# Kernel tuning notes

Hardware: AMD Instinct MI355X
Metric: run time of the kernel (lower is better)

Reference implementation:

```python
import jax, jax.numpy as jnp
import numpy as np

N_HEAD = 16
N_EMBD = 1024
B, T = 4, 1024


def setup_inputs() -> dict:
    key = jax.random.key(0)
    ks = jax.random.split(key, 8)
    hs = N_EMBD // N_HEAD
    x = jax.random.normal(ks[0], (B, T, N_EMBD), dtype=jnp.float32)
    # previous-layer attention load per token, ~O(1/T) like a softmax column mean
    refractory_state = jax.random.uniform(ks[1], (B, T), dtype=jnp.float32) / T
    s_attn = 1.0 / np.sqrt(N_EMBD)
    W_attn = jax.random.normal(ks[2], (N_EMBD, 3 * N_EMBD), dtype=jnp.float32) * s_attn
    b_attn = jnp.zeros((3 * N_EMBD,), dtype=jnp.float32)
    W_proj = jax.random.normal(ks[3], (N_EMBD, N_EMBD), dtype=jnp.float32) * s_attn
    b_proj = jnp.zeros((N_EMBD,), dtype=jnp.float32)
    # learnable LIF params, init per module (lif_mode='refractory')
    threshold = jnp.full((N_HEAD,), 0.01, dtype=jnp.float32)
    leak = jnp.full((N_HEAD,), 2.0, dtype=jnp.float32)
    steepness = jnp.full((N_HEAD,), 2.0, dtype=jnp.float32)
    ref_strength = jnp.full((N_HEAD,), -2.0, dtype=jnp.float32)
    cross_w = jnp.full((N_HEAD,), -2.0, dtype=jnp.float32)
    return {
        "x": x, "refractory_state": refractory_state,
        "W_attn": W_attn, "b_attn": b_attn,
        "W_proj": W_proj, "b_proj": b_proj,
        "threshold": threshold, "leak": leak, "steepness": steepness,
        "ref_strength": ref_strength, "cross_w": cross_w,
    }


def reference(x, refractory_state, W_attn, b_attn, W_proj, b_proj,
              threshold, leak, steepness, ref_strength, cross_w):
    Bq, Tq, C = x.shape
    H = N_HEAD
    hs = C // H
    qkv = x @ W_attn + b_attn                     # [B,T,3C]
    q, k, v = jnp.split(qkv, 3, axis=-1)
    q = q.reshape(Bq, Tq, H, hs).transpose(0, 2, 1, 3)  # [B,H,T,hs]
    k = k.reshape(Bq, Tq, H, hs).transpose(0, 2, 1, 3)
    v = v.reshape(Bq, Tq, H, hs).transpose(0, 2, 1, 3)

    att = jnp.einsum('bhqd,bhkd->bhqk', q, k) * (1.0 / jnp.sqrt(jnp.asarray(hs, x.dtype)))
    causal = jnp.tril(jnp.ones((Tq, Tq), dtype=bool))
    att = jnp.where(causal[None, None], att, -jnp.inf)
    probs = jax.nn.softmax(att, axis=-1)          # [B,H,T,T]

    thr = (jnp.abs(threshold) * 0.1)[None, :, None, None]
    lk = jax.nn.sigmoid(leak)[None, :, None, None]
    st = jax.nn.softplus(steepness)[None, :, None, None]
    # refractory: column load over queries + cross-layer load
    column_load = probs.mean(axis=-2, keepdims=True)          # [B,H,1,T]
    eff_thr = thr + jax.nn.softplus(ref_strength)[None, :, None, None] * column_load
    eff_thr = eff_thr + jax.nn.sigmoid(cross_w)[None, :, None, None] * refractory_state[:, None, None, :]

    fire = jax.nn.sigmoid(st * (probs - eff_thr))
    lif_w = fire + lk * (1.0 - fire)
    mod = probs * lif_w
    mod = mod / (mod.sum(axis=-1, keepdims=True) + 1e-8)
    new_refractory = mod.mean(axis=1).mean(axis=-2)           # [B,T]

    y = jnp.einsum('bhqk,bhkd->bhqd', mod, v)
    y = y.transpose(0, 2, 1, 3).reshape(Bq, Tq, C)
    y = y @ W_proj + b_proj
    return y, new_refractory
```

## Files before the change

### kernel.cpp

```cpp
#include <hip/hip_runtime.h>
#include <math.h>

#define B_  4
#define T_  1024
#define C_  1024
#define H_  16
#define HS_ 64
#define K2E 0.1803368801f
#define LOG2E 1.44269504f

typedef _Float16 f16;
typedef _Float16 f16x8 __attribute__((ext_vector_type(8)));
typedef float f32x4 __attribute__((ext_vector_type(4)));

#define MFMA16(a,b,c) __builtin_amdgcn_mfma_f32_16x16x32_f16(a,b,c,0,0,0)
#define EXP2(x) __builtin_amdgcn_exp2f(x)
#define RCP(x)  __builtin_amdgcn_rcpf(x)

__device__ __forceinline__ float qsum_(float v){
    v += __shfl_xor(v,1,64); v += __shfl_xor(v,2,64);
    v += __shfl_xor(v,4,64); v += __shfl_xor(v,8,64);
    return v;
}
__device__ __forceinline__ float sigmoidf_(float x){ return 1.0f/(1.0f + __expf(-x)); }
__device__ __forceinline__ float softplusf_(float x){ return fmaxf(x, 0.0f) + log1pf(__expf(-fabsf(x))); }

__global__ __launch_bounds__(256) void conv_f16_k(
    const float* __restrict__ in, f16* __restrict__ out, int n8)
{
    int i = blockIdx.x*256 + threadIdx.x;
    if (i < n8){
        const float4* p = (const float4*)in + (size_t)i*2;
        float4 a = p[0], b = p[1];
        f16x8 o;
        o[0]=(f16)a.x; o[1]=(f16)a.y; o[2]=(f16)a.z; o[3]=(f16)a.w;
        o[4]=(f16)b.x; o[5]=(f16)b.y; o[6]=(f16)b.z; o[7]=(f16)b.w;
        *((f16x8*)out + i) = o;
    }
}

__global__ __launch_bounds__(256) void transpose_f16_k(
    const float* __restrict__ in, f16* __restrict__ out, int K, int N)
{
    __shared__ float tl[32][33];
    const int n0 = blockIdx.x*32, k0 = blockIdx.y*32;
    const int c = threadIdx.x & 31, r4 = threadIdx.x >> 5;
    #pragma unroll
    for (int i=0;i<4;i++){
        int r = r4*4 + i;
        tl[r][c] = in[(size_t)(k0+r)*N + n0 + c];
    }
    __syncthreads();
    #pragma unroll
    for (int i=0;i<4;i++){
        int r = r4*4 + i;
        out[(size_t)(n0+r)*K + k0 + c] = (f16)tl[c][r];
    }
}

#define CT_STRIDE 132
__global__ __launch_bounds__(256) void gemm_qkv_k(
    const f16* __restrict__ A, const f16* __restrict__ Bt,
    const float* __restrict__ bias,
    f16* __restrict__ Qh, f16* __restrict__ Kh, f16* __restrict__ Vt)
{
    __shared__ __align__(16) f16 smem[128*CT_STRIDE];
    f16* Al = smem;
    f16* Bl = smem + 4096;
    f16* Ct = smem;
    const int tid = threadIdx.x;
    const int lane = tid & 63, wave = tid >> 6;
    const int lx = lane & 15, quad = lane >> 4;
    const int wm = wave & 1, wn = wave >> 1;
    const int m0 = blockIdx.y*128, n0 = blockIdx.x*128;
    f32x4 acc[4][4];
    #pragma unroll
    for (int i=0;i<4;i++){
        #pragma unroll
        for (int j=0;j<4;j++){ acc[i][j][0]=0.f;acc[i][j][1]=0.f;acc[i][j][2]=0.f;acc[i][j][3]=0.f; }
    }
    f16x8 ra[2], rb[2];
    #pragma unroll
    for (int i=0;i<2;i++){
        int c = i*4 + wave;
        ra[i] = *(const f16x8*)(A  + (size_t)(m0 + c*16 + lx)*1024 + quad*8);
        rb[i] = *(const f16x8*)(Bt + (size_t)(n0 + c*16 + lx)*1024 + quad*8);
    }
    for (int k0=0; k0<1024; k0+=32){
        __syncthreads();
        #pragma unroll
        for (int i=0;i<2;i++){
            int c = i*4 + wave;
            *(f16x8*)&Al[c*512 + quad*128 + lx*8] = ra[i];
            *(f16x8*)&Bl[c*512 + quad*128 + lx*8] = rb[i];
        }
        __syncthreads();
        if (k0 + 32 < 1024){
            #pragma unroll
            for (int i=0;i<2;i++){
                int c = i*4 + wave;
                ra[i] = *(const f16x8*)(A  + (size_t)(m0 + c*16 + lx)*1024 + k0+32 + quad*8);
                rb[i] = *(const f16x8*)(Bt + (size_t)(n0 + c*16 + lx)*1024 + k0+32 + quad*8);
            }
        }
        f16x8 af[4], bf[4];
        #pragma unroll
        for (int mt=0;mt<4;mt++) af[mt] = *(const f16x8*)&Al[(wm*4+mt)*512 + quad*128 + lx*8];
        #pragma unroll
        for (int nt=0;nt<4;nt++) bf[nt] = *(const f16x8*)&Bl[(wn*4+nt)*512 + quad*128 + lx*8];
        #pragma unroll
        for (int mt=0;mt<4;mt++){
            #pragma unroll
            for (int nt=0;nt<4;nt++)
                acc[mt][nt] = MFMA16(af[mt], bf[nt], acc[mt][nt]);
        }
    }
    __syncthreads();
    #pragma unroll
    for (int mt=0;mt<4;mt++){
        #pragma unroll
        for (int nt=0;nt<4;nt++){
            int n_loc = wn*64 + nt*16 + lx;
            float bv = bias[n0 + n_loc];
            #pragma unroll
            for (int r=0;r<4;r++){
                int m_loc = wm*64 + mt*16 + quad*4 + r;
                Ct[m_loc*CT_STRIDE + n_loc] = (f16)(acc[mt][nt][r] + bv);
            }
        }
    }
    __syncthreads();
    const int bb = m0 >> 10;
    if (n0 < 2048){
        for (int it=0; it<8; it++){
            int row = it*32 + wave*8 + (lane>>3);
            int ch  = lane & 7;
            int m_loc = row >> 1, half = row & 1;
            f16x8 v = *(const f16x8*)&Ct[m_loc*CT_STRIDE + half*64 + ch*8];
            int n = n0 + half*64;
            int which = n >> 10, cc = n & 1023, h = cc >> 6;
            int t = (m0 + m_loc) & 1023;
            f16* dst = (which==0) ? Qh : Kh;
            *(f16x8*)(dst + ((size_t)(bb*16+h)*1024 + t)*64 + ch*8) = v;
        }
    } else {
        for (int it=0; it<8; it++){
            int drow = it*16 + wave*4 + (lane>>4);
            int ch   = lane & 15;
            int cc = (n0 + drow) & 1023;
            int h = cc >> 6, d = cc & 63;
            f16 tmp[8];
            #pragma unroll
            for (int j=0;j<8;j++) tmp[j] = Ct[(ch*8+j)*CT_STRIDE + drow];
            int t = (m0 + ch*8) & 1023;
            *(f16x8*)(Vt + ((size_t)(bb*16+h)*64 + d)*1024 + t) = *(f16x8*)tmp;
        }
    }
}

__global__ __launch_bounds__(256) void gemm_proj_k(
    const f16* __restrict__ A, const f16* __restrict__ Bt,
    const float* __restrict__ bias, float* __restrict__ out)
{
    __shared__ __align__(16) f16 Al[8*512];
    __shared__ __align__(16) f16 Bl[4*512];
    const int tid = threadIdx.x;
    const int lane = tid & 63, wave = tid >> 6;
    const int lx = lane & 15, quad = lane >> 4;
    const int wm = wave & 1, wn = wave >> 1;
    const int m0 = blockIdx.y*128, n0 = blockIdx.x*64;
    f32x4 acc[4][2];
    #pragma unroll
    for (int i=0;i<4;i++){
        #pragma unroll
        for (int j=0;j<2;j++){ acc[i][j][0]=0.f;acc[i][j][1]=0.f;acc[i][j][2]=0.f;acc[i][j][3]=0.f; }
    }
    f16x8 ra[2], rb;
    #pragma unroll
    for (int i=0;i<2;i++)
        ra[i] = *(const f16x8*)(A + (size_t)(m0 + (i*4+wave)*16 + lx)*1024 + quad*8);
    rb = *(const f16x8*)(Bt + (size_t)(n0 + wave*16 + lx)*1024 + quad*8);
    for (int k0=0; k0<1024; k0+=32){
        __syncthreads();
        #pragma unroll
        for (int i=0;i<2;i++)
            *(f16x8*)&Al[(i*4+wave)*512 + quad*128 + lx*8] = ra[i];
        *(f16x8*)&Bl[wave*512 + quad*128 + lx*8] = rb;
        __syncthreads();
        if (k0 + 32 < 1024){
            #pragma unroll
            for (int i=0;i<2;i++)
                ra[i] = *(const f16x8*)(A + (size_t)(m0 + (i*4+wave)*16 + lx)*1024 + k0+32 + quad*8);
            rb = *(const f16x8*)(Bt + (size_t)(n0 + wave*16 + lx)*1024 + k0+32 + quad*8);
        }
        f16x8 af[4], bf[2];
        #pragma unroll
        for (int mt=0;mt<4;mt++) af[mt] = *(const f16x8*)&Al[(wm*4+mt)*512 + quad*128 + lx*8];
        #pragma unroll
        for (int nt=0;nt<2;nt++) bf[nt] = *(const f16x8*)&Bl[(wn*2+nt)*512 + quad*128 + lx*8];
        #pragma unroll
        for (int mt=0;mt<4;mt++){
            #pragma unroll
            for (int nt=0;nt<2;nt++)
                acc[mt][nt] = MFMA16(af[mt], bf[nt], acc[mt][nt]);
        }
    }
    #pragma unroll
    for (int mt=0;mt<4;mt++){
        #pragma unroll
        for (int nt=0;nt<2;nt++){
            int n = n0 + wn*32 + nt*16 + lx;
            float bv = bias[n];
            #pragma unroll
            for (int r=0;r<4;r++){
                int m = m0 + wm*64 + mt*16 + quad*4 + r;
                out[(size_t)m*1024 + n] = acc[mt][nt][r] + bv;
            }
        }
    }
}

__global__ __launch_bounds__(256) void attn_stats_k(
    const f16* __restrict__ Qh, const f16* __restrict__ Kh,
    float* __restrict__ rowl, float* __restrict__ colp)
{
    __shared__ __align__(16) f16 Kl[4096];
    __shared__ float colacc[64];
    const int tid = threadIdx.x;
    const int lane = tid & 63, wave = tid >> 6;
    const int lx = lane & 15, quad = lane >> 4;
    const int g  = 15 - (blockIdx.x >> 6);
    const int bh = blockIdx.x & 63;
    const int qpos = wave*16 + quad*4;
    const size_t kbase = (size_t)bh*1024*64;

    const size_t qoff = ((size_t)bh*1024 + g*64 + wave*16 + lx)*64;
    f16x8 aq0 = *(const f16x8*)(Qh + qoff + quad*8);
    f16x8 aq1 = *(const f16x8*)(Qh + qoff + 32 + quad*8);

    f16x8 rk[2];
    #pragma unroll
    for (int i=0;i<2;i++){
        int u = i*4+wave, c = u&3, kh = u>>2;
        rk[i] = *(const f16x8*)(Kh + kbase + (size_t)(c*16+lx)*64 + kh*32 + quad*8);
    }

    float ls[4] = {0.f,0.f,0.f,0.f};
    for (int kt=0; kt<=g; kt++){
        __syncthreads();
        #pragma unroll
        for (int i=0;i<2;i++){
            int u = i*4+wave, c = u&3, kh = u>>2;
            *(f16x8*)&Kl[c*1024 + kh*512 + quad*128 + lx*8] = rk[i];
        }
        __syncthreads();
        if (kt < g){
            #pragma unroll
            for (int i=0;i<2;i++){
                int u = i*4+wave, c = u&3, kh = u>>2;
                rk[i] = *(const f16x8*)(Kh + kbase + (size_t)((kt+1)*64 + c*16+lx)*64 + kh*32 + quad*8);
            }
        }
        const bool diag = (kt == g);
        #pragma unroll
        for (int nt=0;nt<4;nt++){
            f32x4 sc = {0.f,0.f,0.f,0.f};
            f16x8 b0 = *(const f16x8*)&Kl[nt*1024 + quad*128 + lx*8];
            f16x8 b1 = *(const f16x8*)&Kl[nt*1024 + 512 + quad*128 + lx*8];
            sc = MFMA16(aq0, b0, sc);
            sc = MFMA16(aq1, b1, sc);
            #pragma unroll
            for (int r=0;r<4;r++){
                float sv = sc[r];
                if (diag && (nt*16+lx) > (qpos + r)) sv = -1e4f;
                ls[r] += EXP2(sv*K2E);
            }
        }
    }
    float invl[4];
    #pragma unroll
    for (int r=0;r<4;r++){
        float l = qsum_(ls[r]);
        if (lx == 0) rowl[(size_t)bh*1024 + g*64 + qpos + r] = l;
        invl[r] = RCP(l);
    }

    #pragma unroll
    for (int i=0;i<2;i++){
        int u = i*4+wave, c = u&3, kh = u>>2;
        rk[i] = *(const f16x8*)(Kh + kbase + (size_t)(c*16+lx)*64 + kh*32 + quad*8);
    }
    for (int kt=0; kt<=g; kt++){
        __syncthreads();
        #pragma unroll
        for (int i=0;i<2;i++){
            int u = i*4+wave, c = u&3, kh = u>>2;
            *(f16x8*)&Kl[c*1024 + kh*512 + quad*128 + lx*8] = rk[i];
        }
        if (tid < 64) colacc[tid] = 0.f;
        __syncthreads();
        if (kt < g){
            #pragma unroll
            for (int i=0;i<2;i++){
                int u = i*4+wave, c = u&3, kh = u>>2;
                rk[i] = *(const f16x8*)(Kh + kbase + (size_t)((kt+1)*64 + c*16+lx)*64 + kh*32 + quad*8);
            }
        }
        const bool diag = (kt == g);
        #pragma unroll
        for (int nt=0;nt<4;nt++){
            f32x4 sc = {0.f,0.f,0.f,0.f};
            f16x8 b0 = *(const f16x8*)&Kl[nt*1024 + quad*128 + lx*8];
            f16x8 b1 = *(const f16x8*)&Kl[nt*1024 + 512 + quad*128 + lx*8];
            sc = MFMA16(aq0, b0, sc);
            sc = MFMA16(aq1, b1, sc);
            float csum = 0.f;
            #pragma unroll
            for (int r=0;r<4;r++){
                float sv = sc[r];
                if (diag && (nt*16+lx) > (qpos + r)) sv = -1e4f;
                csum += EXP2(sv*K2E) * invl[r];
            }
            csum += __shfl_xor(csum,16,64); csum += __shfl_xor(csum,32,64);
            if (quad == 0) atomicAdd(&colacc[nt*16+lx], csum);
        }
        __syncthreads();
        if (tid < 64) atomicAdd(&colp[(size_t)bh*1024 + kt*64 + tid], colacc[tid]);
    }
}

__global__ __launch_bounds__(256) void attn_apply_k(
    const f16* __restrict__ Qh, const f16* __restrict__ Kh, const f16* __restrict__ Vt,
    const float* __restrict__ rowl,
    const float* __restrict__ colp, const float* __restrict__ refr,
    const float* __restrict__ threshold, const float* __restrict__ leak,
    const float* __restrict__ steepness, const float* __restrict__ ref_strength,
    const float* __restrict__ cross_w,
    f16* __restrict__ Yh, float* __restrict__ racc)
{
    __shared__ __align__(16) f16 Kl[4096];
    __shared__ __align__(16) f16 Vl[4096];
    __shared__ __align__(16) f16 Pl[4][16*72];
    __shared__ float eb[1024];
    __shared__ float colacc[64];
    const int tid = threadIdx.x;
    const int lane = tid & 63, wave = tid >> 6;
    const int lx = lane & 15, quad = lane >> 4;
    const int g  = 15 - (blockIdx.x >> 6);
    const int bh = blockIdx.x & 63;
    const int b  = bh >> 4, h = bh & 15;
    const int qpos = wave*16 + quad*4;
    const size_t kbase = (size_t)bh*1024*64;

    const float thr = fabsf(threshold[h])*0.1f;
    const float lk  = sigmoidf_(leak[h]);
    const float st2 = softplusf_(steepness[h]) * LOG2E;
    const float sprT= softplusf_(ref_strength[h]) * (1.0f/T_);
    const float cw  = sigmoidf_(cross_w[h]);
    const float Alk = 1.f - lk;

    {
        float4 cp = *(const float4*)(colp + (size_t)bh*1024 + tid*4);
        float4 rf = *(const float4*)(refr + (size_t)b*1024 + tid*4);
        eb[tid*4+0] = thr + sprT*cp.x + cw*rf.x;
        eb[tid*4+1] = thr + sprT*cp.y + cw*rf.y;
        eb[tid*4+2] = thr + sprT*cp.z + cw*rf.z;
        eb[tid*4+3] = thr + sprT*cp.w + cw*rf.w;
    }

    const size_t qoff = ((size_t)bh*1024 + g*64 + wave*16 + lx)*64;
    f16x8 aq0 = *(const f16x8*)(Qh + qoff + quad*8);
    f16x8 aq1 = *(const f16x8*)(Qh + qoff + 32 + quad*8);

    float invl[4];
    #pragma unroll
    for (int r=0;r<4;r++)
        invl[r] = RCP(rowl[(size_t)bh*1024 + g*64 + qpos + r]);

    f32x4 y[4];
    #pragma unroll
    for (int i=0;i<4;i++){ y[i][0]=0.f;y[i][1]=0.f;y[i][2]=0.f;y[i][3]=0.f; }
    float Dp[4] = {0.f,0.f,0.f,0.f};

    f16x8 rk[2], rv[2];
    #pragma unroll
    for (int i=0;i<2;i++){
        int u = i*4+wave, c = u&3, kh = u>>2;
        rk[i] = *(const f16x8*)(Kh + kbase + (size_t)(c*16+lx)*64 + kh*32 + quad*8);
        rv[i] = *(const f16x8*)(Vt + kbase + (size_t)(c*16+lx)*1024 + kh*32 + quad*8);
    }

    for (int kt=0; kt<=g; kt++){
        __syncthreads();
        #pragma unroll
        for (int i=0;i<2;i++){
            int u = i*4+wave, c = u&3, kh = u>>2;
            *(f16x8*)&Kl[c*1024 + kh*512 + quad*128 + lx*8] = rk[i];
            *(f16x8*)&Vl[c*1024 + kh*512 + quad*128 + lx*8] = rv[i];
        }
        __syncthreads();
        if (kt < g){
            #pragma unroll
            for (int i=0;i<2;i++){
                int u = i*4+wave, c = u&3, kh = u>>2;
                rk[i] = *(const f16x8*)(Kh + kbase + (size_t)((kt+1)*64 + c*16+lx)*64 + kh*32 + quad*8);
                rv[i] = *(const f16x8*)(Vt + kbase + (size_t)(c*16+lx)*1024 + (kt+1)*64 + kh*32 + quad*8);
            }
        }
        const bool diag = (kt == g);
        #pragma unroll
        for (int nt=0;nt<4;nt++){
            f32x4 sc = {0.f,0.f,0.f,0.f};
            f16x8 b0 = *(const f16x8*)&Kl[nt*1024 + quad*128 + lx*8];
            f16x8 b1 = *(const f16x8*)&Kl[nt*1024 + 512 + quad*128 + lx*8];
            sc = MFMA16(aq0, b0, sc);
            sc = MFMA16(aq1, b1, sc);
            float ec = st2 * eb[kt*64 + nt*16 + lx];
            #pragma unroll
            for (int r=0;r<4;r++){
                float sv = sc[r];
                if (diag && (nt*16+lx) > (qpos + r)) sv = -1e4f;
                float p = EXP2(sv*K2E) * invl[r];
                float e2 = EXP2(ec - st2*p);
                float fire = RCP(1.f + e2);
                float pw = p * (lk + Alk*fire);
                Dp[r] += pw;
                Pl[wave][(quad*4+r)*72 + nt*16 + lx] = (f16)pw;
            }
        }
        f16x8 ap0 = *(const f16x8*)&Pl[wave][lx*72 + quad*8];
        f16x8 ap1 = *(const f16x8*)&Pl[wave][lx*72 + 32 + quad*8];
        #pragma unroll
        for (int dt=0;dt<4;dt++){
            f16x8 bv0 = *(const f16x8*)&Vl[dt*1024 + quad*128 + lx*8];
            f16x8 bv1 = *(const f16x8*)&Vl[dt*1024 + 512 + quad*128 + lx*8];
            y[dt] = MFMA16(ap0, bv0, y[dt]);
            y[dt] = MFMA16(ap1, bv1, y[dt]);
        }
    }
    float invD[4];
    #pragma unroll
    for (int r=0;r<4;r++) invD[r] = RCP(qsum_(Dp[r]) + 1e-8f);
    #pragma unroll
    for (int dt=0;dt<4;dt++){
        #pragma unroll
        for (int r=0;r<4;r++)
            Pl[wave][(quad*4+r)*72 + dt*16 + lx] = (f16)(y[dt][r]*invD[r]);
    }
    #pragma unroll
    for (int it=0; it<2; it++){
        int q = it*8 + (lane>>3), ch = lane & 7;
        f16x8 v = *(const f16x8*)&Pl[wave][q*72 + ch*8];
        *(f16x8*)(Yh + (size_t)(b*1024 + g*64 + wave*16 + q)*1024 + h*64 + ch*8) = v;
    }

    #pragma unroll
    for (int i=0;i<2;i++){
        int u = i*4+wave, c = u&3, kh = u>>2;
        rk[i] = *(const f16x8*)(Kh + kbase + (size_t)(c*16+lx)*64 + kh*32 + quad*8);
    }
    for (int kt=0; kt<=g; kt++){
        __syncthreads();
        #pragma unroll
        for (int i=0;i<2;i++){
            int u = i*4+wave, c = u&3, kh = u>>2;
            *(f16x8*)&Kl[c*1024 + kh*512 + quad*128 + lx*8] = rk[i];
        }
        if (tid < 64) colacc[tid] = 0.f;
        __syncthreads();
        if (kt < g){
            #pragma unroll
            for (int i=0;i<2;i++){
                int u = i*4+wave, c = u&3, kh = u>>2;
                rk[i] = *(const f16x8*)(Kh + kbase + (size_t)((kt+1)*64 + c*16+lx)*64 + kh*32 + quad*8);
            }
        }
        const bool diag = (kt == g);
        #pragma unroll
        for (int nt=0;nt<4;nt++){
            f32x4 sc = {0.f,0.f,0.f,0.f};
            f16x8 b0 = *(const f16x8*)&Kl[nt*1024 + quad*128 + lx*8];
            f16x8 b1 = *(const f16x8*)&Kl[nt*1024 + 512 + quad*128 + lx*8];
            sc = MFMA16(aq0, b0, sc);
            sc = MFMA16(aq1, b1, sc);
            float ec = st2 * eb[kt*64 + nt*16 + lx];
            float csum = 0.f;
            #pragma unroll
            for (int r=0;r<4;r++){
                float sv = sc[r];
                if (diag && (nt*16+lx) > (qpos + r)) sv = -1e4f;
                float p = EXP2(sv*K2E) * invl[r];
                float e2 = EXP2(ec - st2*p);
                float fire = RCP(1.f + e2);
                csum += p * (lk + Alk*fire) * invD[r];
            }
            csum += __shfl_xor(csum,16,64); csum += __shfl_xor(csum,32,64);
            if (quad == 0) atomicAdd(&colacc[nt*16+lx], csum);
        }
        __syncthreads();
        if (tid < 64) atomicAdd(&racc[(size_t)b*1024 + kt*64 + tid], colacc[tid]);
    }
}

__global__ __launch_bounds__(256) void finish_refr_k(
    const float* __restrict__ racc, float* __restrict__ out)
{
    int i = blockIdx.x*256 + threadIdx.x;
    if (i < B_*T_) out[i] = racc[i] * (1.0f/(H_*T_));
}

extern "C" void kernel_launch(void* const* d_in, const int* in_sizes, int n_in,
                              void* d_out, int out_size, void* d_ws, size_t ws_size,
                              hipStream_t stream) {
    (void)in_sizes; (void)n_in; (void)out_size; (void)ws_size;
    const float* x           = (const float*)d_in[0];
    const float* refr        = (const float*)d_in[1];
    const float* W_attn      = (const float*)d_in[2];
    const float* b_attn      = (const float*)d_in[3];
    const float* W_proj      = (const float*)d_in[4];
    const float* b_proj      = (const float*)d_in[5];
    const float* threshold   = (const float*)d_in[6];
    const float* leak        = (const float*)d_in[7];
    const float* steepness   = (const float*)d_in[8];
    const float* ref_strength= (const float*)d_in[9];
    const float* cross_w     = (const float*)d_in[10];
    float* out = (float*)d_out;

    char* ws = (char*)d_ws;
    f16* x_h = (f16*)ws;                       ws += (size_t)4096*1024*2;
    f16* WaT = (f16*)ws;                       ws += (size_t)3072*1024*2;
    f16* WpT = (f16*)ws;                       ws += (size_t)1024*1024*2;
    f16* Qh  = (f16*)ws;                       ws += (size_t)64*1024*64*2;
    f16* Kh  = (f16*)ws;                       ws += (size_t)64*1024*64*2;
    f16* Vt  = (f16*)ws;                       ws += (size_t)64*64*1024*2;
    f16* Yh  = (f16*)ws;                       ws += (size_t)4096*1024*2;
    float* rowl = (float*)ws;                  ws += (size_t)65536*4;
    float* colp = (float*)ws;                  ws += (size_t)65536*4;
    float* racc = (float*)ws;                  ws += (size_t)4096*4;

    hipMemsetAsync(colp, 0, 65536*sizeof(float), stream);
    hipMemsetAsync(racc, 0, 4096*sizeof(float), stream);

    conv_f16_k<<<dim3(2048), dim3(256), 0, stream>>>(x, x_h, 4096*1024/8);
    transpose_f16_k<<<dim3(96,32), dim3(256), 0, stream>>>(W_attn, WaT, 1024, 3072);
    transpose_f16_k<<<dim3(32,32), dim3(256), 0, stream>>>(W_proj, WpT, 1024, 1024);
    gemm_qkv_k<<<dim3(24,32), dim3(256), 0, stream>>>(x_h, WaT, b_attn, Qh, Kh, Vt);
    attn_stats_k<<<dim3(1024), dim3(256), 0, stream>>>(Qh, Kh, rowl, colp);
    attn_apply_k<<<dim3(1024), dim3(256), 0, stream>>>(
        Qh, Kh, Vt, rowl, colp, refr,
        threshold, leak, steepness, ref_strength, cross_w, Yh, racc);
    gemm_proj_k<<<dim3(16,32), dim3(256), 0, stream>>>(Yh, WpT, b_proj, out);
    finish_refr_k<<<dim3(16), dim3(256), 0, stream>>>(racc, out + (size_t)B_*T_*C_);
}
```

Before: 289.8 us.

## Double-buffer LDS tiles, fuse prep kernels, and batch column atomics

Merges the conversion, both weight transposes and the workspace zeroing into one prep kernel, replacing two memsets and three launches. The finish kernel is folded into the projection GEMM as an extra block. The GEMMs and attention loops now double-buffer their LDS tiles with two-deep register prefetch, cutting syncs per iteration from two to one. Per-block column sums go into a full-length shared accumulator and are flushed to global atomics once at the end instead of every tile. The costs are more LDS per block, which may reduce occupancy, and the fused proj kernel reads racc without any visible ordering guarantee relative to attn_apply, though stream order should cover it.

```diff
diff --git a/kernel.cpp b/kernel.cpp
--- a/kernel.cpp
+++ b/kernel.cpp
@@ -25,36 +25,44 @@
 __device__ __forceinline__ float sigmoidf_(float x){ return 1.0f/(1.0f + __expf(-x)); }
 __device__ __forceinline__ float softplusf_(float x){ return fmaxf(x, 0.0f) + log1pf(__expf(-fabsf(x))); }
 
-__global__ __launch_bounds__(256) void conv_f16_k(
-    const float* __restrict__ in, f16* __restrict__ out, int n8)
+__global__ __launch_bounds__(256) void prep_k(
+    const float* __restrict__ x, const float* __restrict__ Wa,
+    const float* __restrict__ Wp,
+    f16* __restrict__ x_h, f16* __restrict__ WaT, f16* __restrict__ WpT,
+    float* __restrict__ zbase)
 {
-    int i = blockIdx.x*256 + threadIdx.x;
-    if (i < n8){
-        const float4* p = (const float4*)in + (size_t)i*2;
+    __shared__ float tl[32][33];
+    const int bid = blockIdx.x, tid = threadIdx.x;
+    if (bid < 2048){
+        int i = bid*256 + tid;
+        const float4* p = (const float4*)x + (size_t)i*2;
         float4 a = p[0], b = p[1];
         f16x8 o;
         o[0]=(f16)a.x; o[1]=(f16)a.y; o[2]=(f16)a.z; o[3]=(f16)a.w;
         o[4]=(f16)b.x; o[5]=(f16)b.y; o[6]=(f16)b.z; o[7]=(f16)b.w;
-        *((f16x8*)out + i) = o;
-    }
-}
-
-__global__ __launch_bounds__(256) void transpose_f16_k(
-    const float* __restrict__ in, f16* __restrict__ out, int K, int N)
-{
-    __shared__ float tl[32][33];
-    const int n0 = blockIdx.x*32, k0 = blockIdx.y*32;
-    const int c = threadIdx.x & 31, r4 = threadIdx.x >> 5;
-    #pragma unroll
-    for (int i=0;i<4;i++){
-        int r = r4*4 + i;
-        tl[r][c] = in[(size_t)(k0+r)*N + n0 + c];
-    }
-    __syncthreads();
-    #pragma unroll
-    for (int i=0;i<4;i++){
-        int r = r4*4 + i;
-        out[(size_t)(n0+r)*K + k0 + c] = (f16)tl[c][r];
+        *((f16x8*)x_h + i) = o;
+    } else if (bid < 5120){
+        int t = bid - 2048;
+        int n0 = (t % 96)*32, k0 = (t / 96)*32;
+        const int c = tid & 31, r4 = tid >> 5;
+        #pragma unroll
+        for (int i=0;i<4;i++){ int r = r4*4+i; tl[r][c] = Wa[(size_t)(k0+r)*3072 + n0 + c]; }
+        __syncthreads();
+        #pragma unroll
+        for (int i=0;i<4;i++){ int r = r4*4+i; WaT[(size_t)(n0+r)*1024 + k0 + c] = (f16)tl[c][r]; }
+    } else if (bid < 6144){
+        int t = bid - 5120;
+        int n0 = (t & 31)*32, k0 = (t >> 5)*32;
+        const int c = tid & 31, r4 = tid >> 5;
+        #pragma unroll
+        for (int i=0;i<4;i++){ int r = r4*4+i; tl[r][c] = Wp[(size_t)(k0+r)*1024 + n0 + c]; }
+        __syncthreads();
+        #pragma unroll
+        for (int i=0;i<4;i++){ int r = r4*4+i; WpT[(size_t)(n0+r)*1024 + k0 + c] = (f16)tl[c][r]; }
+    } else {
+        int idx = (bid - 6144)*256 + tid;
+        float4 z; z.x=0.f; z.y=0.f; z.z=0.f; z.w=0.f;
+        ((float4*)zbase)[idx] = z;
     }
 }
 
@@ -64,58 +72,72 @@
     const float* __restrict__ bias,
     f16* __restrict__ Qh, f16* __restrict__ Kh, f16* __restrict__ Vt)
 {
-    __shared__ __align__(16) f16 smem[128*CT_STRIDE];
-    f16* Al = smem;
-    f16* Bl = smem + 4096;
-    f16* Ct = smem;
+    __shared__ __align__(16) f16 smem[16896];
     const int tid = threadIdx.x;
     const int lane = tid & 63, wave = tid >> 6;
     const int lx = lane & 15, quad = lane >> 4;
     const int wm = wave & 1, wn = wave >> 1;
     const int m0 = blockIdx.y*128, n0 = blockIdx.x*128;
+    const f16* Ap = A  + (size_t)m0*1024;
+    const f16* Bp = Bt + (size_t)n0*1024;
     f32x4 acc[4][4];
     #pragma unroll
     for (int i=0;i<4;i++){
         #pragma unroll
         for (int j=0;j<4;j++){ acc[i][j][0]=0.f;acc[i][j][1]=0.f;acc[i][j][2]=0.f;acc[i][j][3]=0.f; }
     }
-    f16x8 ra[2], rb[2];
+    f16x8 ra[2][2], rb[2][2];
     #pragma unroll
     for (int i=0;i<2;i++){
         int c = i*4 + wave;
-        ra[i] = *(const f16x8*)(A  + (size_t)(m0 + c*16 + lx)*1024 + quad*8);
-        rb[i] = *(const f16x8*)(Bt + (size_t)(n0 + c*16 + lx)*1024 + quad*8);
-    }
-    for (int k0=0; k0<1024; k0+=32){
-        __syncthreads();
-        #pragma unroll
-        for (int i=0;i<2;i++){
-            int c = i*4 + wave;
-            *(f16x8*)&Al[c*512 + quad*128 + lx*8] = ra[i];
-            *(f16x8*)&Bl[c*512 + quad*128 + lx*8] = rb[i];
-        }
-        __syncthreads();
-        if (k0 + 32 < 1024){
+        ra[0][i] = *(const f16x8*)(Ap + (size_t)(c*16+lx)*1024 + quad*8);
+        rb[0][i] = *(const f16x8*)(Bp + (size_t)(c*16+lx)*1024 + quad*8);
+    }
+    #pragma unroll
+    for (int i=0;i<2;i++){
+        int c = i*4 + wave;
+        *(f16x8*)&smem[c*512 + quad*128 + lx*8]        = ra[0][i];
+        *(f16x8*)&smem[4096 + c*512 + quad*128 + lx*8] = rb[0][i];
+    }
+    #pragma unroll
+    for (int i=0;i<2;i++){
+        int c = i*4 + wave;
+        ra[1][i] = *(const f16x8*)(Ap + (size_t)(c*16+lx)*1024 + 32 + quad*8);
+        rb[1][i] = *(const f16x8*)(Bp + (size_t)(c*16+lx)*1024 + 32 + quad*8);
+    }
+    __syncthreads();
+    for (int it=0; it<32; it++){
+        const int cur = (it&1)*8192, nxt = 8192 - cur, s = it&1;
+        if (it < 30){
             #pragma unroll
             for (int i=0;i<2;i++){
                 int c = i*4 + wave;
-                ra[i] = *(const f16x8*)(A  + (size_t)(m0 + c*16 + lx)*1024 + k0+32 + quad*8);
-                rb[i] = *(const f16x8*)(Bt + (size_t)(n0 + c*16 + lx)*1024 + k0+32 + quad*8);
+                ra[s][i] = *(const f16x8*)(Ap + (size_t)(c*16+lx)*1024 + (it+2)*32 + quad*8);
+                rb[s][i] = *(const f16x8*)(Bp + (size_t)(c*16+lx)*1024 + (it+2)*32 + quad*8);
+            }
+        }
+        if (it < 31){
+            #pragma unroll
+            for (int i=0;i<2;i++){
+                int c = i*4 + wave;
+                *(f16x8*)&smem[nxt + c*512 + quad*128 + lx*8]        = ra[s^1][i];
+                *(f16x8*)&smem[nxt + 4096 + c*512 + quad*128 + lx*8] = rb[s^1][i];
             }
         }
         f16x8 af[4], bf[4];
         #pragma unroll
-        for (int mt=0;mt<4;mt++) af[mt] = *(const f16x8*)&Al[(wm*4+mt)*512 + quad*128 + lx*8];
-        #pragma unroll
-        for (int nt=0;nt<4;nt++) bf[nt] = *(const f16x8*)&Bl[(wn*4+nt)*512 + quad*128 + lx*8];
+        for (int mt=0;mt<4;mt++) af[mt] = *(const f16x8*)&smem[cur + (wm*4+mt)*512 + quad*128 + lx*8];
+        #pragma unroll
+        for (int nt=0;nt<4;nt++) bf[nt] = *(const f16x8*)&smem[cur + 4096 + (wn*4+nt)*512 + quad*128 + lx*8];
         #pragma unroll
         for (int mt=0;mt<4;mt++){
             #pragma unroll
             for (int nt=0;nt<4;nt++)
                 acc[mt][nt] = MFMA16(af[mt], bf[nt], acc[mt][nt]);
         }
-    }
-    __syncthreads();
+        __syncthreads();
+    }
+    f16* Ct = smem;
     #pragma unroll
     for (int mt=0;mt<4;mt++){
         #pragma unroll
@@ -160,50 +182,72 @@
 
 __global__ __launch_bounds__(256) void gemm_proj_k(
     const f16* __restrict__ A, const f16* __restrict__ Bt,
-    const float* __restrict__ bias, float* __restrict__ out)
+    const float* __restrict__ bias, float* __restrict__ out,
+    const float* __restrict__ racc)
 {
-    __shared__ __align__(16) f16 Al[8*512];
-    __shared__ __align__(16) f16 Bl[4*512];
+    if (blockIdx.x == 512){
+        float* oref = out + (size_t)B_*T_*C_;
+        #pragma unroll
+        for (int j=0;j<16;j++){
+            int idx = j*256 + threadIdx.x;
+            oref[idx] = racc[idx] * (1.0f/(H_*T_));
+        }
+        return;
+    }
+    __shared__ __align__(16) f16 smem[12288];
     const int tid = threadIdx.x;
     const int lane = tid & 63, wave = tid >> 6;
     const int lx = lane & 15, quad = lane >> 4;
     const int wm = wave & 1, wn = wave >> 1;
-    const int m0 = blockIdx.y*128, n0 = blockIdx.x*64;
+    const int m0 = (blockIdx.x >> 4)*128, n0 = (blockIdx.x & 15)*64;
+    const f16* Ap = A  + (size_t)m0*1024;
+    const f16* Bp = Bt + (size_t)n0*1024;
     f32x4 acc[4][2];
     #pragma unroll
     for (int i=0;i<4;i++){
         #pragma unroll
         for (int j=0;j<2;j++){ acc[i][j][0]=0.f;acc[i][j][1]=0.f;acc[i][j][2]=0.f;acc[i][j][3]=0.f; }
     }
-    f16x8 ra[2], rb;
+    f16x8 ra[2][2], rb[2];
     #pragma unroll
     for (int i=0;i<2;i++)
-        ra[i] = *(const f16x8*)(A + (size_t)(m0 + (i*4+wave)*16 + lx)*1024 + quad*8);
-    rb = *(const f16x8*)(Bt + (size_t)(n0 + wave*16 + lx)*1024 + quad*8);
-    for (int k0=0; k0<1024; k0+=32){
-        __syncthreads();
-        #pragma unroll
-        for (int i=0;i<2;i++)
-            *(f16x8*)&Al[(i*4+wave)*512 + quad*128 + lx*8] = ra[i];
-        *(f16x8*)&Bl[wave*512 + quad*128 + lx*8] = rb;
-        __syncthreads();
-        if (k0 + 32 < 1024){
+        ra[0][i] = *(const f16x8*)(Ap + (size_t)((i*4+wave)*16+lx)*1024 + quad*8);
+    rb[0] = *(const f16x8*)(Bp + (size_t)(wave*16+lx)*1024 + quad*8);
+    #pragma unroll
+    for (int i=0;i<2;i++)
+        *(f16x8*)&smem[(i*4+wave)*512 + quad*128 + lx*8] = ra[0][i];
+    *(f16x8*)&smem[4096 + wave*512 + quad*128 + lx*8] = rb[0];
+    #pragma unroll
+    for (int i=0;i<2;i++)
+        ra[1][i] = *(const f16x8*)(Ap + (size_t)((i*4+wave)*16+lx)*1024 + 32 + quad*8);
+    rb[1] = *(const f16x8*)(Bp + (size_t)(wave*16+lx)*1024 + 32 + quad*8);
+    __syncthreads();
+    for (int it=0; it<32; it++){
+        const int cur = (it&1)*6144, nxt = 6144 - cur, s = it&1;
+        if (it < 30){
             #pragma unroll
             for (int i=0;i<2;i++)
-                ra[i] = *(const f16x8*)(A + (size_t)(m0 + (i*4+wave)*16 + lx)*1024 + k0+32 + quad*8);
-            rb = *(const f16x8*)(Bt + (size_t)(n0 + wave*16 + lx)*1024 + k0+32 + quad*8);
+                ra[s][i] = *(const f16x8*)(Ap + (size_t)((i*4+wave)*16+lx)*1024 + (it+2)*32 + quad*8);
+            rb[s] = *(const f16x8*)(Bp + (size_t)(wave*16+lx)*1024 + (it+2)*32 + quad*8);
+        }
+        if (it < 31){
+            #pragma unroll
+            for (int i=0;i<2;i++)
+                *(f16x8*)&smem[nxt + (i*4+wave)*512 + quad*128 + lx*8] = ra[s^1][i];
+            *(f16x8*)&smem[nxt + 4096 + wave*512 + quad*128 + lx*8] = rb[s^1];
         }
         f16x8 af[4], bf[2];
         #pragma unroll
-        for (int mt=0;mt<4;mt++) af[mt] = *(const f16x8*)&Al[(wm*4+mt)*512 + quad*128 + lx*8];
-        #pragma unroll
-        for (int nt=0;nt<2;nt++) bf[nt] = *(const f16x8*)&Bl[(wn*2+nt)*512 + quad*128 + lx*8];
+        for (int mt=0;mt<4;mt++) af[mt] = *(const f16x8*)&smem[cur + (wm*4+mt)*512 + quad*128 + lx*8];
+        #pragma unroll
+        for (int nt=0;nt<2;nt++) bf[nt] = *(const f16x8*)&smem[cur + 4096 + (wn*2+nt)*512 + quad*128 + lx*8];
         #pragma unroll
         for (int mt=0;mt<4;mt++){
             #pragma unroll
             for (int nt=0;nt<2;nt++)
                 acc[mt][nt] = MFMA16(af[mt], bf[nt], acc[mt][nt]);
         }
+        __syncthreads();
     }
     #pragma unroll
     for (int mt=0;mt<4;mt++){
@@ -224,49 +268,54 @@
     const f16* __restrict__ Qh, const f16* __restrict__ Kh,
     float* __restrict__ rowl, float* __restrict__ colp)
 {
-    __shared__ __align__(16) f16 Kl[4096];
-    __shared__ float colacc[64];
+    __shared__ __align__(16) f16 Kl[8192];
+    __shared__ float cacc[1024];
     const int tid = threadIdx.x;
     const int lane = tid & 63, wave = tid >> 6;
     const int lx = lane & 15, quad = lane >> 4;
     const int g  = 15 - (blockIdx.x >> 6);
     const int bh = blockIdx.x & 63;
     const int qpos = wave*16 + quad*4;
-    const size_t kbase = (size_t)bh*1024*64;
+    const size_t kbase = (size_t)bh*65536;
+
+    for (int i=tid; i<1024; i+=256) cacc[i] = 0.f;
 
     const size_t qoff = ((size_t)bh*1024 + g*64 + wave*16 + lx)*64;
     f16x8 aq0 = *(const f16x8*)(Qh + qoff + quad*8);
     f16x8 aq1 = *(const f16x8*)(Qh + qoff + 32 + quad*8);
 
-    f16x8 rk[2];
-    #pragma unroll
-    for (int i=0;i<2;i++){
-        int u = i*4+wave, c = u&3, kh = u>>2;
-        rk[i] = *(const f16x8*)(Kh + kbase + (size_t)(c*16+lx)*64 + kh*32 + quad*8);
-    }
-
+    f16x8 rk[2][2];
+    #pragma unroll
+    for (int i=0;i<2;i++){ int u=i*4+wave, cc=u&3, kh=u>>2;
+        rk[0][i] = *(const f16x8*)(Kh + kbase + (size_t)(cc*16+lx)*64 + kh*32 + quad*8); }
+    #pragma unroll
+    for (int i=0;i<2;i++){ int u=i*4+wave, cc=u&3, kh=u>>2;
+        *(f16x8*)&Kl[cc*1024 + kh*512 + quad*128 + lx*8] = rk[0][i]; }
+    if (g >= 1){
+        #pragma unroll
+        for (int i=0;i<2;i++){ int u=i*4+wave, cc=u&3, kh=u>>2;
+            rk[1][i] = *(const f16x8*)(Kh + kbase + (size_t)(64 + cc*16+lx)*64 + kh*32 + quad*8); }
+    }
+    __syncthreads();
     float ls[4] = {0.f,0.f,0.f,0.f};
     for (int kt=0; kt<=g; kt++){
-        __syncthreads();
-        #pragma unroll
-        for (int i=0;i<2;i++){
-            int u = i*4+wave, c = u&3, kh = u>>2;
-            *(f16x8*)&Kl[c*1024 + kh*512 + quad*128 + lx*8] = rk[i];
-        }
-        __syncthreads();
-        if (kt < g){
-            #pragma unroll
-            for (int i=0;i<2;i++){
-                int u = i*4+wave, c = u&3, kh = u>>2;
-                rk[i] = *(const f16x8*)(Kh + kbase + (size_t)((kt+1)*64 + c*16+lx)*64 + kh*32 + quad*8);
-            }
+        const int cur = (kt&1)*4096, nxt = 4096 - cur, s = kt&1;
+        if (kt+2 <= g){
+            #pragma unroll
+            for (int i=0;i<2;i++){ int u=i*4+wave, cc=u&3, kh=u>>2;
+                rk[s][i] = *(const f16x8*)(Kh + kbase + (size_t)((kt+2)*64 + cc*16+lx)*64 + kh*32 + quad*8); }
+        }
+        if (kt+1 <= g){
+            #pragma unroll
+            for (int i=0;i<2;i++){ int u=i*4+wave, cc=u&3, kh=u>>2;
+                *(f16x8*)&Kl[nxt + cc*1024 + kh*512 + quad*128 + lx*8] = rk[s^1][i]; }
         }
         const bool diag = (kt == g);
         #pragma unroll
         for (int nt=0;nt<4;nt++){
             f32x4 sc = {0.f,0.f,0.f,0.f};
-            f16x8 b0 = *(const f16x8*)&Kl[nt*1024 + quad*128 + lx*8];
-            f16x8 b1 = *(const f16x8*)&Kl[nt*1024 + 512 + quad*128 + lx*8];
+            f16x8 b0 = *(const f16x8*)&Kl[cur + nt*1024 + quad*128 + lx*8];
+            f16x8 b1 = *(const f16x8*)&Kl[cur + nt*1024 + 512 + quad*128 + lx*8];
             sc = MFMA16(aq0, b0, sc);
             sc = MFMA16(aq1, b1, sc);
             #pragma unroll
@@ -276,6 +325,7 @@
                 ls[r] += EXP2(sv*K2E);
             }
         }
+        __syncthreads();
     }
     float invl[4];
     #pragma unroll
@@ -284,34 +334,36 @@
         if (lx == 0) rowl[(size_t)bh*1024 + g*64 + qpos + r] = l;
         invl[r] = RCP(l);
     }
-
-    #pragma unroll
-    for (int i=0;i<2;i++){
-        int u = i*4+wave, c = u&3, kh = u>>2;
-        rk[i] = *(const f16x8*)(Kh + kbase + (size_t)(c*16+lx)*64 + kh*32 + quad*8);
-    }
+    #pragma unroll
+    for (int i=0;i<2;i++){ int u=i*4+wave, cc=u&3, kh=u>>2;
+        rk[0][i] = *(const f16x8*)(Kh + kbase + (size_t)(cc*16+lx)*64 + kh*32 + quad*8); }
+    #pragma unroll
+    for (int i=0;i<2;i++){ int u=i*4+wave, cc=u&3, kh=u>>2;
+        *(f16x8*)&Kl[cc*1024 + kh*512 + quad*128 + lx*8] = rk[0][i]; }
+    if (g >= 1){
+        #pragma unroll
+        for (int i=0;i<2;i++){ int u=i*4+wave, cc=u&3, kh=u>>2;
+            rk[1][i] = *(const f16x8*)(Kh + kbase + (size_t)(64 + cc*16+lx)*64 + kh*32 + quad*8); }
+    }
+    __syncthreads();
     for (int kt=0; kt<=g; kt++){
-        __syncthreads();
-        #pragma unroll
-        for (int i=0;i<2;i++){
-            int u = i*4+wave, c = u&3, kh = u>>2;
-            *(f16x8*)&Kl[c*1024 + kh*512 + quad*128 + lx*8] = rk[i];
-        }
-        if (tid < 64) colacc[tid] = 0.f;
-        __syncthreads();
-        if (kt < g){
-            #pragma unroll
-            for (int i=0;i<2;i++){
-                int u = i*4+wave, c = u&3, kh = u>>2;
-                rk[i] = *(const f16x8*)(Kh + kbase + (size_t)((kt+1)*64 + c*16+lx)*64 + kh*32 + quad*8);
-            }
+        const int cur = (kt&1)*4096, nxt = 4096 - cur, s = kt&1;
+        if (kt+2 <= g){
+            #pragma unroll
+            for (int i=0;i<2;i++){ int u=i*4+wave, cc=u&3, kh=u>>2;
+                rk[s][i] = *(const f16x8*)(Kh + kbase + (size_t)((kt+2)*64 + cc*16+lx)*64 + kh*32 + quad*8); }
+        }
+        if (kt+1 <= g){
+            #pragma unroll
+            for (int i=0;i<2;i++){ int u=i*4+wave, cc=u&3, kh=u>>2;
+                *(f16x8*)&Kl[nxt + cc*1024 + kh*512 + quad*128 + lx*8] = rk[s^1][i]; }
         }
         const bool diag = (kt == g);
         #pragma unroll
         for (int nt=0;nt<4;nt++){
             f32x4 sc = {0.f,0.f,0.f,0.f};
-            f16x8 b0 = *(const f16x8*)&Kl[nt*1024 + quad*128 + lx*8];
-            f16x8 b1 = *(const f16x8*)&Kl[nt*1024 + 512 + quad*128 + lx*8];
+            f16x8 b0 = *(const f16x8*)&Kl[cur + nt*1024 + quad*128 + lx*8];
+            f16x8 b1 = *(const f16x8*)&Kl[cur + nt*1024 + 512 + quad*128 + lx*8];
             sc = MFMA16(aq0, b0, sc);
             sc = MFMA16(aq1, b1, sc);
             float csum = 0.f;
@@ -322,11 +374,12 @@
                 csum += EXP2(sv*K2E) * invl[r];
             }
             csum += __shfl_xor(csum,16,64); csum += __shfl_xor(csum,32,64);
-            if (quad == 0) atomicAdd(&colacc[nt*16+lx], csum);
-        }
-        __syncthreads();
-        if (tid < 64) atomicAdd(&colp[(size_t)bh*1024 + kt*64 + tid], colacc[tid]);
-    }
+            if (quad == 0) atomicAdd(&cacc[kt*64 + nt*16 + lx], csum);
+        }
+        __syncthreads();
+    }
+    for (int i=tid; i<(g+1)*64; i+=256)
+        atomicAdd(&colp[(size_t)bh*1024 + i], cacc[i]);
 }
 
 __global__ __launch_bounds__(256) void attn_apply_k(
@@ -338,11 +391,11 @@
     const float* __restrict__ cross_w,
     f16* __restrict__ Yh, float* __restrict__ racc)
 {
-    __shared__ __align__(16) f16 Kl[4096];
-    __shared__ __align__(16) f16 Vl[4096];
+    __shared__ __align__(16) f16 Kl[8192];
+    __shared__ __align__(16) f16 Vl[8192];
     __shared__ __align__(16) f16 Pl[4][16*72];
     __shared__ float eb[1024];
-    __shared__ float colacc[64];
+    __shared__ float cacc[1024];
     const int tid = threadIdx.x;
     const int lane = tid & 63, wave = tid >> 6;
     const int lx = lane & 15, quad = lane >> 4;
@@ -350,7 +403,7 @@
     const int bh = blockIdx.x & 63;
     const int b  = bh >> 4, h = bh & 15;
     const int qpos = wave*16 + quad*4;
-    const size_t kbase = (size_t)bh*1024*64;
+    const size_t kbase = (size_t)bh*65536;
 
     const float thr = fabsf(threshold[h])*0.1f;
     const float lk  = sigmoidf_(leak[h]);
@@ -362,11 +415,12 @@
     {
         float4 cp = *(const float4*)(colp + (size_t)bh*1024 + tid*4);
         float4 rf = *(const float4*)(refr + (size_t)b*1024 + tid*4);
-        eb[tid*4+0] = thr + sprT*cp.x + cw*rf.x;
-        eb[tid*4+1] = thr + sprT*cp.y + cw*rf.y;
-        eb[tid*4+2] = thr + sprT*cp.z + cw*rf.z;
-        eb[tid*4+3] = thr + sprT*cp.w + cw*rf.w;
-    }
+        eb[tid*4+0] = st2*(thr + sprT*cp.x + cw*rf.x);
+        eb[tid*4+1] = st2*(thr + sprT*cp.y + cw*rf.y);
+        eb[tid*4+2] = st2*(thr + sprT*cp.z + cw*rf.z);
+        eb[tid*4+3] = st2*(thr + sprT*cp.w + cw*rf.w);
+    }
+    for (int i=tid; i<1024; i+=256) cacc[i] = 0.f;
 
     const size_t qoff = ((size_t)bh*1024 + g*64 + wave*16 + lx)*64;
     f16x8 aq0 = *(const f16x8*)(Qh + qoff + quad*8);
@@ -382,47 +436,51 @@
     for (int i=0;i<4;i++){ y[i][0]=0.f;y[i][1]=0.f;y[i][2]=0.f;y[i][3]=0.f; }
     float Dp[4] = {0.f,0.f,0.f,0.f};
 
-    f16x8 rk[2], rv[2];
-    #pragma unroll
-    for (int i=0;i<2;i++){
-        int u = i*4+wave, c = u&3, kh = u>>2;
-        rk[i] = *(const f16x8*)(Kh + kbase + (size_t)(c*16+lx)*64 + kh*32 + quad*8);
-        rv[i] = *(const f16x8*)(Vt + kbase + (size_t)(c*16+lx)*1024 + kh*32 + quad*8);
-    }
-
+    f16x8 rk[2][2], rv[2][2];
+    #pragma unroll
+    for (int i=0;i<2;i++){ int u=i*4+wave, cc=u&3, kh=u>>2;
+        rk[0][i] = *(const f16x8*)(Kh + kbase + (size_t)(cc*16+lx)*64 + kh*32 + quad*8);
+        rv[0][i] = *(const f16x8*)(Vt + kbase + (size_t)(cc*16+lx)*1024 + kh*32 + quad*8); }
+    #pragma unroll
+    for (int i=0;i<2;i++){ int u=i*4+wave, cc=u&3, kh=u>>2;
+        *(f16x8*)&Kl[cc*1024 + kh*512 + quad*128 + lx*8] = rk[0][i];
+        *(f16x8*)&Vl[cc*1024 + kh*512 + quad*128 + lx*8] = rv[0][i]; }
+    if (g >= 1){
+        #pragma unroll
+        for (int i=0;i<2;i++){ int u=i*4+wave, cc=u&3, kh=u>>2;
+            rk[1][i] = *(const f16x8*)(Kh + kbase + (size_t)(64 + cc*16+lx)*64 + kh*32 + quad*8);
+            rv[1][i] = *(const f16x8*)(Vt + kbase + (size_t)(cc*16+lx)*1024 + 64 + kh*32 + quad*8); }
+    }
+    __syncthreads();
     for (int kt=0; kt<=g; kt++){
-        __syncthreads();
-        #pragma unroll
-        for (int i=0;i<2;i++){
-            int u = i*4+wave, c = u&3, kh = u>>2;
-            *(f16x8*)&Kl[c*1024 + kh*512 + quad*128 + lx*8] = rk[i];
-            *(f16x8*)&Vl[c*1024 + kh*512 + quad*128 + lx*8] = rv[i];
-        }
-        __syncthreads();
-        if (kt < g){
-            #pragma unroll
-            for (int i=0;i<2;i++){
-                int u = i*4+wave, c = u&3, kh = u>>2;
-                rk[i] = *(const f16x8*)(Kh + kbase + (size_t)((kt+1)*64 + c*16+lx)*64 + kh*32 + quad*8);
-                rv[i] = *(const f16x8*)(Vt + kbase + (size_t)(c*16+lx)*1024 + (kt+1)*64 + kh*32 + quad*8);
-            }
+        const int cur = (kt&1)*4096, nxt = 4096 - cur, s = kt&1;
+        if (kt+2 <= g){
+            #pragma unroll
+            for (int i=0;i<2;i++){ int u=i*4+wave, cc=u&3, kh=u>>2;
+                rk[s][i] = *(const f16x8*)(Kh + kbase + (size_t)((kt+2)*64 + cc*16+lx)*64 + kh*32 + quad*8);
+                rv[s][i] = *(const f16x8*)(Vt + kbase + (size_t)(cc*16+lx)*1024 + (kt+2)*64 + kh*32 + quad*8); }
+        }
+        if (kt+1 <= g){
+            #pragma unroll
+            for (int i=0;i<2;i++){ int u=i*4+wave, cc=u&3, kh=u>>2;
+                *(f16x8*)&Kl[nxt + cc*1024 + kh*512 + quad*128 + lx*8] = rk[s^1][i];
+                *(f16x8*)&Vl[nxt + cc*1024 + kh*512 + quad*128 + lx*8] = rv[s^1][i]; }
         }
         const bool diag = (kt == g);
         #pragma unroll
         for (int nt=0;nt<4;nt++){
             f32x4 sc = {0.f,0.f,0.f,0.f};
-            f16x8 b0 = *(const f16x8*)&Kl[nt*1024 + quad*128 + lx*8];
-            f16x8 b1 = *(const f16x8*)&Kl[nt*1024 + 512 + quad*128 + lx*8];
+            f16x8 b0 = *(const f16x8*)&Kl[cur + nt*1024 + quad*128 + lx*8];
+            f16x8 b1 = *(const f16x8*)&Kl[cur + nt*1024 + 512 + quad*128 + lx*8];
             sc = MFMA16(aq0, b0, sc);
             sc = MFMA16(aq1, b1, sc);
-            float ec = st2 * eb[kt*64 + nt*16 + lx];
+            float ec = eb[kt*64 + nt*16 + lx];
             #pragma unroll
             for (int r=0;r<4;r++){
                 float sv = sc[r];
                 if (diag && (nt*16+lx) > (qpos + r)) sv = -1e4f;
                 float p = EXP2(sv*K2E) * invl[r];
-                float e2 = EXP2(ec - st2*p);
-                float fire = RCP(1.f + e2);
+                float fire = RCP(1.f + EXP2(ec - st2*p));
                 float pw = p * (lk + Alk*fire);
                 Dp[r] += pw;
                 Pl[wave][(quad*4+r)*72 + nt*16 + lx] = (f16)pw;
@@ -432,11 +490,12 @@
         f16x8 ap1 = *(const f16x8*)&Pl[wave][lx*72 + 32 + quad*8];
         #pragma unroll
         for (int dt=0;dt<4;dt++){
-            f16x8 bv0 = *(const f16x8*)&Vl[dt*1024 + quad*128 + lx*8];
-            f16x8 bv1 = *(const f16x8*)&Vl[dt*1024 + 512 + quad*128 + lx*8];
+            f16x8 bv0 = *(const f16x8*)&Vl[cur + dt*1024 + quad*128 + lx*8];
+            f16x8 bv1 = *(const f16x8*)&Vl[cur + dt*1024 + 512 + quad*128 + lx*8];
             y[dt] = MFMA16(ap0, bv0, y[dt]);
             y[dt] = MFMA16(ap1, bv1, y[dt]);
         }
+        __syncthreads();
     }
     float invD[4];
     #pragma unroll
@@ -455,58 +514,54 @@
     }
 
     #pragma unroll
-    for (int i=0;i<2;i++){
-        int u = i*4+wave, c = u&3, kh = u>>2;
-        rk[i] = *(const f16x8*)(Kh + kbase + (size_t)(c*16+lx)*64 + kh*32 + quad*8);
-    }
+    for (int i=0;i<2;i++){ int u=i*4+wave, cc=u&3, kh=u>>2;
+        rk[0][i] = *(const f16x8*)(Kh + kbase + (size_t)(cc*16+lx)*64 + kh*32 + quad*8); }
+    #pragma unroll
+    for (int i=0;i<2;i++){ int u=i*4+wave, cc=u&3, kh=u>>2;
+        *(f16x8*)&Kl[cc*1024 + kh*512 + quad*128 + lx*8] = rk[0][i]; }
+    if (g >= 1){
+        #pragma unroll
+        for (int i=0;i<2;i++){ int u=i*4+wave, cc=u&3, kh=u>>2;
+            rk[1][i] = *(const f16x8*)(Kh + kbase + (size_t)(64 + cc*16+lx)*64 + kh*32 + quad*8); }
+    }
+    __syncthreads();
     for (int kt=0; kt<=g; kt++){
-        __syncthreads();
-        #pragma unroll
-        for (int i=0;i<2;i++){
-            int u = i*4+wave, c = u&3, kh = u>>2;
-            *(f16x8*)&Kl[c*1024 + kh*512 + quad*128 + lx*8] = rk[i];
-        }
-        if (tid < 64) colacc[tid] = 0.f;
-        __syncthreads();
-        if (kt < g){
-            #pragma unroll
-            for (int i=0;i<2;i++){
-                int u = i*4+wave, c = u&3, kh = u>>2;
-                rk[i] = *(const f16x8*)(Kh + kbase + (size_t)((kt+1)*64 + c*16+lx)*64 + kh*32 + quad*8);
-            }
+        const int cur = (kt&1)*4096, nxt = 4096 - cur, s = kt&1;
+        if (kt+2 <= g){
+            #pragma unroll
+            for (int i=0;i<2;i++){ int u=i*4+wave, cc=u&3, kh=u>>2;
+                rk[s][i] = *(const f16x8*)(Kh + kbase + (size_t)((kt+2)*64 + cc*16+lx)*64 + kh*32 + quad*8); }
+        }
+        if (kt+1 <= g){
+            #pragma unroll
+            for (int i=0;i<2;i++){ int u=i*4+wave, cc=u&3, kh=u>>2;
+                *(f16x8*)&Kl[nxt + cc*1024 + kh*512 + quad*128 + lx*8] = rk[s^1][i]; }
         }
         const bool diag = (kt == g);
         #pragma unroll
         for (int nt=0;nt<4;nt++){
             f32x4 sc = {0.f,0.f,0.f,0.f};
-            f16x8 b0 = *(const f16x8*)&Kl[nt*1024 + quad*128 + lx*8];
-            f16x8 b1 = *(const f16x8*)&Kl[nt*1024 + 512 + quad*128 + lx*8];
+            f16x8 b0 = *(const f16x8*)&Kl[cur + nt*1024 + quad*128 + lx*8];
+            f16x8 b1 = *(const f16x8*)&Kl[cur + nt*1024 + 512 + quad*128 + lx*8];
             sc = MFMA16(aq0, b0, sc);
             sc = MFMA16(aq1, b1, sc);
-            float ec = st2 * eb[kt*64 + nt*16 + lx];
+            float ec = eb[kt*64 + nt*16 + lx];
             float csum = 0.f;
             #pragma unroll
             for (int r=0;r<4;r++){
                 float sv = sc[r];
                 if (diag && (nt*16+lx) > (qpos + r)) sv = -1e4f;
                 float p = EXP2(sv*K2E) * invl[r];
-                float e2 = EXP2(ec - st2*p);
-                float fire = RCP(1.f + e2);
+                float fire = RCP(1.f + EXP2(ec - st2*p));
                 csum += p * (lk + Alk*fire) * invD[r];
             }
             csum += __shfl_xor(csum,16,64); csum += __shfl_xor(csum,32,64);
-            if (quad == 0) atomicAdd(&colacc[nt*16+lx], csum);
-        }
-        __syncthreads();
-        if (tid < 64) atomicAdd(&racc[(size_t)b*1024 + kt*64 + tid], colacc[tid]);
-    }
-}
-
-__global__ __launch_bounds__(256) void finish_refr_k(
-    const float* __restrict__ racc, float* __restrict__ out)
-{
-    int i = blockIdx.x*256 + threadIdx.x;
-    if (i < B_*T_) out[i] = racc[i] * (1.0f/(H_*T_));
+            if (quad == 0) atomicAdd(&cacc[kt*64 + nt*16 + lx], csum);
+        }
+        __syncthreads();
+    }
+    for (int i=tid; i<(g+1)*64; i+=256)
+        atomicAdd(&racc[(size_t)b*1024 + i], cacc[i]);
 }
 
 extern "C" void kernel_launch(void* const* d_in, const int* in_sizes, int n_in,
@@ -538,17 +593,11 @@
     float* colp = (float*)ws;                  ws += (size_t)65536*4;
     float* racc = (float*)ws;                  ws += (size_t)4096*4;
 
-    hipMemsetAsync(colp, 0, 65536*sizeof(float), stream);
-    hipMemsetAsync(racc, 0, 4096*sizeof(float), stream);
-
-    conv_f16_k<<<dim3(2048), dim3(256), 0, stream>>>(x, x_h, 4096*1024/8);
-    transpose_f16_k<<<dim3(96,32), dim3(256), 0, stream>>>(W_attn, WaT, 1024, 3072);
-    transpose_f16_k<<<dim3(32,32), dim3(256), 0, stream>>>(W_proj, WpT, 1024, 1024);
+    prep_k<<<dim3(6212), dim3(256), 0, stream>>>(x, W_attn, W_proj, x_h, WaT, WpT, colp);
     gemm_qkv_k<<<dim3(24,32), dim3(256), 0, stream>>>(x_h, WaT, b_attn, Qh, Kh, Vt);
     attn_stats_k<<<dim3(1024), dim3(256), 0, stream>>>(Qh, Kh, rowl, colp);
     attn_apply_k<<<dim3(1024), dim3(256), 0, stream>>>(
         Qh, Kh, Vt, rowl, colp, refr,
         threshold, leak, steepness, ref_strength, cross_w, Yh, racc);
-    gemm_proj_k<<<dim3(16,32), dim3(256), 0, stream>>>(Yh, WpT, b_proj, out);
-    finish_refr_k<<<dim3(16), dim3(256), 0, stream>>>(racc, out + (size_t)B_*T_*C_);
+    gemm_proj_k<<<dim3(513), dim3(256), 0, stream>>>(Yh, WpT, b_proj, out, racc);
 }
```

New measurement: 1.101 ms. 3.8x slower.
